# Performance work log

Measured on AMD Instinct MI355X. Metric: run time of the kernel, lower is better.

Reference implementation:

```python
import jax, jax.numpy as jnp
import numpy as np

B, N, F0 = 256, 256, 128
LAYER_SIZES = [128, 128, 128]


def setup_inputs() -> dict:
    key = jax.random.key(0)
    ks = jax.random.split(key, 10)
    x = jax.random.normal(ks[0], (B, N, F0), dtype=jnp.float32)
    adj = jax.random.uniform(ks[1], (B, N, N), dtype=jnp.float32)
    adj = 0.5 * (adj + jnp.swapaxes(adj, -1, -2))  # symmetric weighted adjacency
    f0, f1, f2 = LAYER_SIZES
    W1 = jax.random.normal(ks[2], (f0, f1), dtype=jnp.float32) / np.sqrt(f0)
    b1 = jnp.zeros((f1,), dtype=jnp.float32)
    W2 = jax.random.normal(ks[3], (f1, f2), dtype=jnp.float32) / np.sqrt(f1)
    b2 = jnp.zeros((f2,), dtype=jnp.float32)
    Wr = jax.random.normal(ks[4], (2 * f2, f2), dtype=jnp.float32) / np.sqrt(2 * f2)
    br = jnp.zeros((f2,), dtype=jnp.float32)
    return {"x": x, "adj": adj, "W1": W1, "b1": b1, "W2": W2, "b2": b2, "Wr": Wr, "br": br}


def _normalize_adj(adj):
    # DenseGCNConv: set self-loops (diag=1), then D^{-1/2} (A+I) D^{-1/2} with deg clamped to >=1
    n = adj.shape[-1]
    eye = jnp.eye(n, dtype=adj.dtype)
    a = adj * (1.0 - eye) + eye
    d = jnp.maximum(a.sum(axis=-1), 1.0) ** -0.5  # [B, N]
    return d[..., :, None] * a * d[..., None, :]


def reference(x, adj, W1, b1, W2, b2, Wr, br):
    a = _normalize_adj(adj)  # same adj for both layers; normalization is identical per layer
    h = jnp.einsum("bnm,bmf->bnf", a, x @ W1) + b1  # DenseGCNConv layer 1
    h = jnp.einsum("bnm,bmf->bnf", a, h @ W2) + b2  # DenseGCNConv layer 2
    pooled = jnp.concatenate([h.mean(axis=1), h.max(axis=1)], axis=-1)  # [B, 2F]
    return pooled @ Wr + br  # [B, F]
```

## Files before the change

### kernel.cpp

```cpp
#include <hip/hip_runtime.h>
#include <cstddef>


typedef __attribute__((ext_vector_type(8))) short short8;
typedef __attribute__((ext_vector_type(4))) float f32x4;

static __device__ __forceinline__ unsigned short f2bf(float f) {
  unsigned int u = __float_as_uint(f);
  u += 0x7FFFu + ((u >> 16) & 1u);
  return (unsigned short)(u >> 16);
}

static __device__ __forceinline__ f32x4 mfma16(short8 a, short8 b, f32x4 c) {
  return __builtin_amdgcn_mfma_f32_16x16x32_bf16(a, b, c, 0, 0, 0);
}

static __device__ __forceinline__ int byteT(int f, int k) {
  return ((f << 9) + (k << 1)) ^ ((f & 7) << 4);
}
static __device__ __forceinline__ int byteH(int n, int k) {
  return ((n << 8) + (k << 1)) ^ ((n & 7) << 4);
}

__global__ __launch_bounds__(256) void k_deg_conv(
    const float* __restrict__ adj, unsigned short* __restrict__ Abf,
    float* __restrict__ dinv) {
  const int wid = (blockIdx.x << 2) + (threadIdx.x >> 6);
  const int t = threadIdx.x & 63;
  const int row0 = wid << 3;
  const size_t base0 = (size_t)row0 * 256;
  const int c0 = 4 * t;

  float4 v[8];
  #pragma unroll
  for (int r = 0; r < 8; ++r)
    v[r] = *reinterpret_cast<const float4*>(adj + base0 + (size_t)r * 256 + c0);

  float s[8];
  #pragma unroll
  for (int r = 0; r < 8; ++r) {
    const int n = (row0 + r) & 255;
    v[r].x = (n == c0 + 0) ? 1.0f : v[r].x;
    v[r].y = (n == c0 + 1) ? 1.0f : v[r].y;
    v[r].z = (n == c0 + 2) ? 1.0f : v[r].z;
    v[r].w = (n == c0 + 3) ? 1.0f : v[r].w;
    s[r] = (v[r].x + v[r].y) + (v[r].z + v[r].w);
  }
  #pragma unroll
  for (int off = 32; off >= 1; off >>= 1) {
    #pragma unroll
    for (int r = 0; r < 8; ++r) s[r] += __shfl_xor(s[r], off);
  }

  float sel = s[0];
  #pragma unroll
  for (int r = 1; r < 8; ++r) sel = (t == r) ? s[r] : sel;
  if (t < 8) dinv[row0 + t] = rsqrtf(fmaxf(sel, 1.0f));

  #pragma unroll
  for (int r = 0; r < 8; ++r) {
    ushort4 o;
    o.x = f2bf(v[r].x); o.y = f2bf(v[r].y);
    o.z = f2bf(v[r].z); o.w = f2bf(v[r].w);
    *reinterpret_cast<ushort4*>(Abf + base0 + (size_t)r * 256 + c0) = o;
  }
}

__global__ __launch_bounds__(64) void k_packW2(
    const float* __restrict__ W1, const float* __restrict__ W2,
    unsigned short* __restrict__ P1, unsigned short* __restrict__ P2) {
  const float* W = (blockIdx.x < 32) ? W1 : W2;
  unsigned short* P = (blockIdx.x < 32) ? P1 : P2;
  const int bb = blockIdx.x & 31;
  const int ks = bb >> 3;
  const int r = bb & 7;
  const int l = threadIdx.x;
  const int col = r * 16 + (l & 15);
  const int k0 = ks * 32 + ((l >> 4) << 3);
  short8 frag;
  #pragma unroll
  for (int j = 0; j < 8; ++j)
    frag[j] = (short)f2bf(W[(size_t)(k0 + j) * 128 + col]);
  *reinterpret_cast<short8*>(P + ((size_t)((ks * 8 + r) * 64 + l)) * 8) = frag;
}

__global__ __launch_bounds__(512) void k_fused(
    const unsigned short* __restrict__ Abf, const float* __restrict__ x,
    const unsigned short* __restrict__ W1p, const unsigned short* __restrict__ W2p,
    const float* __restrict__ b1, const float* __restrict__ b2,
    const float* __restrict__ Wr, const float* __restrict__ br,
    const float* __restrict__ dinv, float* __restrict__ out) {
  __shared__ __align__(16) char bufA[65536];
  __shared__ __align__(16) char bufB[65536];
  __shared__ float dinv_s[256];

  const int b = blockIdx.x;
  const int tid = threadIdx.x;
  const int w = tid >> 6;
  const int l = tid & 63;
  const int l15 = l & 15;
  const int khalf = (l >> 4) << 3;
  const int qbase = (l >> 4) << 2;
  const int m = (w << 4) + l15;
  const unsigned short* Ab = Abf + ((size_t)b << 16);
  const int n0w = w << 5;

  float4 xa[4];
  {
    const float* xr = x + ((((size_t)b << 8) + m) << 7);
    #pragma unroll
    for (int k = 0; k < 2; ++k) {
      xa[2 * k]     = *reinterpret_cast<const float4*>(xr + (k << 5) + khalf);
      xa[2 * k + 1] = *reinterpret_cast<const float4*>(xr + (k << 5) + khalf + 4);
    }
  }
  if (tid < 256) dinv_s[tid] = dinv[(b << 8) + tid];
  __syncthreads();

  {
    const short8* Wf = reinterpret_cast<const short8*>(W1p);
    {
      const float* xr = x + ((((size_t)b << 8) + m) << 7);
      float4 xb[4];
      #pragma unroll
      for (int ks = 2; ks < 4; ++ks) {
        xb[2 * (ks - 2)]     = *reinterpret_cast<const float4*>(xr + (ks << 5) + khalf);
        xb[2 * (ks - 2) + 1] = *reinterpret_cast<const float4*>(xr + (ks << 5) + khalf + 4);
      }
      f32x4 acc[8];
      #pragma unroll
      for (int r = 0; r < 8; ++r) acc[r] = (f32x4)(0.0f);
      #pragma unroll
      for (int ks = 0; ks < 4; ++ks) {
        const float4 u = (ks < 2) ? xa[2 * ks] : xb[2 * (ks - 2)];
        const float4 vv = (ks < 2) ? xa[2 * ks + 1] : xb[2 * (ks - 2) + 1];
        short8 bf;
        bf[0] = (short)f2bf(u.x);  bf[1] = (short)f2bf(u.y);
        bf[2] = (short)f2bf(u.z);  bf[3] = (short)f2bf(u.w);
        bf[4] = (short)f2bf(vv.x); bf[5] = (short)f2bf(vv.y);
        bf[6] = (short)f2bf(vv.z); bf[7] = (short)f2bf(vv.w);
        #pragma unroll
        for (int r = 0; r < 8; ++r)
          acc[r] = mfma16(Wf[((ks << 3) + r) * 64 + l], bf, acc[r]);
      }
      const float sc = dinv_s[m];
      #pragma unroll
      for (int r = 0; r < 8; ++r)
        #pragma unroll
        for (int q = 0; q < 4; ++q)
          *reinterpret_cast<unsigned short*>(bufA + byteT((r << 4) + qbase + q, m)) =
              f2bf(acc[r][q] * sc);
    }
    {
      const int m1 = m + 128;
      const float* xr = x + ((((size_t)b << 8) + m1) << 7);
      float4 xc[8];
      #pragma unroll
      for (int ks = 0; ks < 4; ++ks) {
        xc[2 * ks]     = *reinterpret_cast<const float4*>(xr + (ks << 5) + khalf);
        xc[2 * ks + 1] = *reinterpret_cast<const float4*>(xr + (ks << 5) + khalf + 4);
      }
      f32x4 acc[8];
      #pragma unroll
      for (int r = 0; r < 8; ++r) acc[r] = (f32x4)(0.0f);
      #pragma unroll
      for (int ks = 0; ks < 4; ++ks) {
        const float4 u = xc[2 * ks], vv = xc[2 * ks + 1];
        short8 bf;
        bf[0] = (short)f2bf(u.x);  bf[1] = (short)f2bf(u.y);
        bf[2] = (short)f2bf(u.z);  bf[3] = (short)f2bf(u.w);
        bf[4] = (short)f2bf(vv.x); bf[5] = (short)f2bf(vv.y);
        bf[6] = (short)f2bf(vv.z); bf[7] = (short)f2bf(vv.w);
        #pragma unroll
        for (int r = 0; r < 8; ++r)
          acc[r] = mfma16(Wf[((ks << 3) + r) * 64 + l], bf, acc[r]);
      }
      const float sc = dinv_s[m1];
      #pragma unroll
      for (int r = 0; r < 8; ++r)
        #pragma unroll
        for (int q = 0; q < 4; ++q)
          *reinterpret_cast<unsigned short*>(bufA + byteT((r << 4) + qbase + q, m1)) =
              f2bf(acc[r][q] * sc);
    }
  }
  __syncthreads();

  {
    float bs[8];
    #pragma unroll
    for (int c = 0; c < 8; ++c) bs[c] = b1[(c << 4) + l15];
    #pragma unroll
    for (int rt = 0; rt < 2; ++rt) {
      const int nb = n0w + (rt << 4);
      short8 af[8];
      #pragma unroll
      for (int ks = 0; ks < 8; ++ks)
        af[ks] = *reinterpret_cast<const short8*>(
            Ab + (size_t)(nb + l15) * 256 + (ks << 5) + khalf);
      f32x4 acc[8];
      #pragma unroll
      for (int c = 0; c < 8; ++c) acc[c] = (f32x4)(0.0f);
      #pragma unroll
      for (int ks = 0; ks < 8; ++ks) {
        const int k0 = (ks << 5) + khalf;
        #pragma unroll
        for (int c = 0; c < 8; ++c) {
          short8 bf = *reinterpret_cast<const short8*>(bufA + byteT((c << 4) + l15, k0));
          acc[c] = mfma16(af[ks], bf, acc[c]);
        }
      }
      #pragma unroll
      for (int q = 0; q < 4; ++q) {
        const int n = nb + qbase + q;
        const float dv = dinv_s[n];
        #pragma unroll
        for (int c = 0; c < 8; ++c)
          *reinterpret_cast<unsigned short*>(bufB + byteH(n, (c << 4) + l15)) =
              f2bf(acc[c][q] * dv + bs[c]);
      }
    }
  }
  __syncthreads();

  {
    const short8* Wf = reinterpret_cast<const short8*>(W2p);
    #pragma unroll
    for (int p = 0; p < 2; ++p) {
      const int mp = (p << 7) + m;
      f32x4 acc[8];
      #pragma unroll
      for (int r = 0; r < 8; ++r) acc[r] = (f32x4)(0.0f);
      #pragma unroll
      for (int ks = 0; ks < 4; ++ks) {
        const int kk = (ks << 5) + khalf;
        short8 hf = *reinterpret_cast<const short8*>(bufB + byteH(mp, kk));
        #pragma unroll
        for (int r = 0; r < 8; ++r)
          acc[r] = mfma16(Wf[((ks << 3) + r) * 64 + l], hf, acc[r]);
      }
      const float sc = dinv_s[mp];
      #pragma unroll
      for (int r = 0; r < 8; ++r)
        #pragma unroll
        for (int q = 0; q < 4; ++q)
          *reinterpret_cast<unsigned short*>(bufA + byteT((r << 4) + qbase + q, mp)) =
              f2bf(acc[r][q] * sc);
    }
  }
  __syncthreads();

  {
    float bs[8], psum[8], pmax[8];
    #pragma unroll
    for (int c = 0; c < 8; ++c) {
      bs[c] = b2[(c << 4) + l15];
      psum[c] = 0.0f; pmax[c] = -1e30f;
    }
    #pragma unroll
    for (int rt = 0; rt < 2; ++rt) {
      const int nb = n0w + (rt << 4);
      short8 af[8];
      #pragma unroll
      for (int ks = 0; ks < 8; ++ks)
        af[ks] = *reinterpret_cast<const short8*>(
            Ab + (size_t)(nb + l15) * 256 + (ks << 5) + khalf);
      f32x4 acc[8];
      #pragma unroll
      for (int c = 0; c < 8; ++c) acc[c] = (f32x4)(0.0f);
      #pragma unroll
      for (int ks = 0; ks < 8; ++ks) {
        const int k0 = (ks << 5) + khalf;
        #pragma unroll
        for (int c = 0; c < 8; ++c) {
          short8 bf = *reinterpret_cast<const short8*>(bufA + byteT((c << 4) + l15, k0));
          acc[c] = mfma16(af[ks], bf, acc[c]);
        }
      }
      #pragma unroll
      for (int q = 0; q < 4; ++q) {
        const int n = nb + qbase + q;
        const float dv = dinv_s[n];
        #pragma unroll
        for (int c = 0; c < 8; ++c) {
          const float v = acc[c][q] * dv + bs[c];
          psum[c] += v;
          pmax[c] = fmaxf(pmax[c], v);
        }
      }
    }
    #pragma unroll
    for (int c = 0; c < 8; ++c) {
      psum[c] += __shfl_xor(psum[c], 16);
      pmax[c] = fmaxf(pmax[c], __shfl_xor(pmax[c], 16));
      psum[c] += __shfl_xor(psum[c], 32);
      pmax[c] = fmaxf(pmax[c], __shfl_xor(pmax[c], 32));
    }
    float* lds_sum = reinterpret_cast<float*>(bufB);
    float* lds_max = lds_sum + 1024;
    float* pooled  = lds_max + 1024;
    float* rp      = pooled + 256;
    if (l < 16) {
      #pragma unroll
      for (int c = 0; c < 8; ++c) {
        lds_sum[(w << 7) + (c << 4) + l] = psum[c];
        lds_max[(w << 7) + (c << 4) + l] = pmax[c];
      }
    }
    __syncthreads();
    if (tid < 128) {
      float s = 0.0f;
      #pragma unroll
      for (int ww = 0; ww < 8; ++ww) s += lds_sum[(ww << 7) + tid];
      pooled[tid] = s * (1.0f / 256.0f);
    } else if (tid < 256) {
      const int f = tid & 127;
      float mx = -1e30f;
      #pragma unroll
      for (int ww = 0; ww < 8; ++ww) mx = fmaxf(mx, lds_max[(ww << 7) + f]);
      pooled[128 + f] = mx;
    }
    __syncthreads();
    {
      const int f = tid & 127, part = tid >> 7;
      const int base = part << 6;
      float o0 = 0.f, o1 = 0.f;
      #pragma unroll 4
      for (int i = 0; i < 64; i += 2) {
        o0 = fmaf(pooled[base + i],     Wr[(base + i) * 128 + f],     o0);
        o1 = fmaf(pooled[base + i + 1], Wr[(base + i + 1) * 128 + f], o1);
      }
      rp[(part << 7) + f] = o0 + o1;
    }
    __syncthreads();
    if (tid < 128) {
      out[(b << 7) + tid] =
          ((rp[tid] + rp[128 + tid]) + (rp[256 + tid] + rp[384 + tid])) + br[tid];
    }
  }
}

extern "C" void kernel_launch(void* const* d_in, const int* in_sizes, int n_in,
                              void* d_out, int out_size, void* d_ws, size_t ws_size,
                              hipStream_t stream) {
  const float* x   = (const float*)d_in[0];
  const float* adj = (const float*)d_in[1];
  const float* W1  = (const float*)d_in[2];
  const float* b1  = (const float*)d_in[3];
  const float* W2  = (const float*)d_in[4];
  const float* b2  = (const float*)d_in[5];
  const float* Wr  = (const float*)d_in[6];
  const float* br  = (const float*)d_in[7];
  float* out = (float*)d_out;

  char* ws = (char*)d_ws;
  unsigned short* Abf  = (unsigned short*)(ws);
  float*          dinv = (float*)(ws + 33554432);
  unsigned short* W1p  = (unsigned short*)(ws + 33816576);
  unsigned short* W2p  = (unsigned short*)(ws + 33849344);

  k_packW2<<<64, 64, 0, stream>>>(W1, W2, W1p, W2p);
  k_deg_conv<<<2048, 256, 0, stream>>>(adj, Abf, dinv);
  k_fused<<<256, 512, 0, stream>>>(Abf, x, W1p, W2p, b1, b2, Wr, br, dinv, out);
}
```

Before: 63.58 us.

## Split fused GCN kernel into per-layer kernels with two blocks per graph

Replaces the single fused kernel (one 512-thread block per graph, 128KB LDS) with two layer kernels that each use two blocks per graph, each block covering half of the output rows. The hidden layer H1 is written to global memory in bf16, and a third small kernel combines the partial mean/max pooling and applies the readout. The aim is to double the block count to 512 and cut LDS per block to 64KB so more blocks fit per CU. The cost is two extra launches, a global round-trip for H1 and the pooling partials, and the X·W projection being recomputed by both halves.

```diff
diff --git a/kernel.cpp b/kernel.cpp
--- a/kernel.cpp
+++ b/kernel.cpp
@@ -17,9 +17,6 @@
 
 static __device__ __forceinline__ int byteT(int f, int k) {
   return ((f << 9) + (k << 1)) ^ ((f & 7) << 4);
-}
-static __device__ __forceinline__ int byteH(int n, int k) {
-  return ((n << 8) + (k << 1)) ^ ((n & 7) << 4);
 }
 
 __global__ __launch_bounds__(256) void k_deg_conv(
@@ -84,17 +81,15 @@
   *reinterpret_cast<short8*>(P + ((size_t)((ks * 8 + r) * 64 + l)) * 8) = frag;
 }
 
-__global__ __launch_bounds__(512) void k_fused(
+__global__ __launch_bounds__(512, 4) void k_layer1(
     const unsigned short* __restrict__ Abf, const float* __restrict__ x,
-    const unsigned short* __restrict__ W1p, const unsigned short* __restrict__ W2p,
-    const float* __restrict__ b1, const float* __restrict__ b2,
-    const float* __restrict__ Wr, const float* __restrict__ br,
-    const float* __restrict__ dinv, float* __restrict__ out) {
-  __shared__ __align__(16) char bufA[65536];
-  __shared__ __align__(16) char bufB[65536];
+    const unsigned short* __restrict__ W1p, const float* __restrict__ b1,
+    const float* __restrict__ dinv, unsigned short* __restrict__ H1) {
+  __shared__ __align__(16) char bufT[65536];
   __shared__ float dinv_s[256];
 
-  const int b = blockIdx.x;
+  const int b = blockIdx.x >> 1;
+  const int half = blockIdx.x & 1;
   const int tid = threadIdx.x;
   const int w = tid >> 6;
   const int l = tid & 63;
@@ -103,57 +98,16 @@
   const int qbase = (l >> 4) << 2;
   const int m = (w << 4) + l15;
   const unsigned short* Ab = Abf + ((size_t)b << 16);
-  const int n0w = w << 5;
-
-  float4 xa[4];
-  {
-    const float* xr = x + ((((size_t)b << 8) + m) << 7);
-    #pragma unroll
-    for (int k = 0; k < 2; ++k) {
-      xa[2 * k]     = *reinterpret_cast<const float4*>(xr + (k << 5) + khalf);
-      xa[2 * k + 1] = *reinterpret_cast<const float4*>(xr + (k << 5) + khalf + 4);
-    }
-  }
+
   if (tid < 256) dinv_s[tid] = dinv[(b << 8) + tid];
   __syncthreads();
 
   {
     const short8* Wf = reinterpret_cast<const short8*>(W1p);
-    {
-      const float* xr = x + ((((size_t)b << 8) + m) << 7);
-      float4 xb[4];
-      #pragma unroll
-      for (int ks = 2; ks < 4; ++ks) {
-        xb[2 * (ks - 2)]     = *reinterpret_cast<const float4*>(xr + (ks << 5) + khalf);
-        xb[2 * (ks - 2) + 1] = *reinterpret_cast<const float4*>(xr + (ks << 5) + khalf + 4);
-      }
-      f32x4 acc[8];
-      #pragma unroll
-      for (int r = 0; r < 8; ++r) acc[r] = (f32x4)(0.0f);
-      #pragma unroll
-      for (int ks = 0; ks < 4; ++ks) {
-        const float4 u = (ks < 2) ? xa[2 * ks] : xb[2 * (ks - 2)];
-        const float4 vv = (ks < 2) ? xa[2 * ks + 1] : xb[2 * (ks - 2) + 1];
-        short8 bf;
-        bf[0] = (short)f2bf(u.x);  bf[1] = (short)f2bf(u.y);
-        bf[2] = (short)f2bf(u.z);  bf[3] = (short)f2bf(u.w);
-        bf[4] = (short)f2bf(vv.x); bf[5] = (short)f2bf(vv.y);
-        bf[6] = (short)f2bf(vv.z); bf[7] = (short)f2bf(vv.w);
-        #pragma unroll
-        for (int r = 0; r < 8; ++r)
-          acc[r] = mfma16(Wf[((ks << 3) + r) * 64 + l], bf, acc[r]);
-      }
-      const float sc = dinv_s[m];
-      #pragma unroll
-      for (int r = 0; r < 8; ++r)
-        #pragma unroll
-        for (int q = 0; q < 4; ++q)
-          *reinterpret_cast<unsigned short*>(bufA + byteT((r << 4) + qbase + q, m)) =
-              f2bf(acc[r][q] * sc);
-    }
-    {
-      const int m1 = m + 128;
-      const float* xr = x + ((((size_t)b << 8) + m1) << 7);
+    #pragma unroll
+    for (int p = 0; p < 2; ++p) {
+      const int mp = (p << 7) + m;
+      const float* xr = x + ((((size_t)b << 8) + mp) << 7);
       float4 xc[8];
       #pragma unroll
       for (int ks = 0; ks < 4; ++ks) {
@@ -175,12 +129,12 @@
         for (int r = 0; r < 8; ++r)
           acc[r] = mfma16(Wf[((ks << 3) + r) * 64 + l], bf, acc[r]);
       }
-      const float sc = dinv_s[m1];
+      const float sc = dinv_s[mp];
       #pragma unroll
       for (int r = 0; r < 8; ++r)
         #pragma unroll
         for (int q = 0; q < 4; ++q)
-          *reinterpret_cast<unsigned short*>(bufA + byteT((r << 4) + qbase + q, m1)) =
+          *reinterpret_cast<unsigned short*>(bufT + byteT((r << 4) + qbase + q, mp)) =
               f2bf(acc[r][q] * sc);
     }
   }
@@ -190,37 +144,58 @@
     float bs[8];
     #pragma unroll
     for (int c = 0; c < 8; ++c) bs[c] = b1[(c << 4) + l15];
-    #pragma unroll
-    for (int rt = 0; rt < 2; ++rt) {
-      const int nb = n0w + (rt << 4);
-      short8 af[8];
-      #pragma unroll
-      for (int ks = 0; ks < 8; ++ks)
-        af[ks] = *reinterpret_cast<const short8*>(
-            Ab + (size_t)(nb + l15) * 256 + (ks << 5) + khalf);
-      f32x4 acc[8];
-      #pragma unroll
-      for (int c = 0; c < 8; ++c) acc[c] = (f32x4)(0.0f);
-      #pragma unroll
-      for (int ks = 0; ks < 8; ++ks) {
-        const int k0 = (ks << 5) + khalf;
-        #pragma unroll
-        for (int c = 0; c < 8; ++c) {
-          short8 bf = *reinterpret_cast<const short8*>(bufA + byteT((c << 4) + l15, k0));
-          acc[c] = mfma16(af[ks], bf, acc[c]);
-        }
-      }
-      #pragma unroll
-      for (int q = 0; q < 4; ++q) {
-        const int n = nb + qbase + q;
-        const float dv = dinv_s[n];
-        #pragma unroll
-        for (int c = 0; c < 8; ++c)
-          *reinterpret_cast<unsigned short*>(bufB + byteH(n, (c << 4) + l15)) =
-              f2bf(acc[c][q] * dv + bs[c]);
-      }
-    }
-  }
+    const int nb = (half << 7) + (w << 4);
+    short8 af[8];
+    #pragma unroll
+    for (int ks = 0; ks < 8; ++ks)
+      af[ks] = *reinterpret_cast<const short8*>(
+          Ab + (size_t)(nb + l15) * 256 + (ks << 5) + khalf);
+    f32x4 acc[8];
+    #pragma unroll
+    for (int c = 0; c < 8; ++c) acc[c] = (f32x4)(0.0f);
+    #pragma unroll
+    for (int ks = 0; ks < 8; ++ks) {
+      const int k0 = (ks << 5) + khalf;
+      #pragma unroll
+      for (int c = 0; c < 8; ++c) {
+        short8 bf = *reinterpret_cast<const short8*>(bufT + byteT((c << 4) + l15, k0));
+        acc[c] = mfma16(af[ks], bf, acc[c]);
+      }
+    }
+    #pragma unroll
+    for (int q = 0; q < 4; ++q) {
+      const int n = nb + qbase + q;
+      const float dv = dinv_s[n];
+      #pragma unroll
+      for (int c = 0; c < 8; ++c)
+        H1[(((size_t)(b << 8) + n) << 7) + (c << 4) + l15] =
+            f2bf(acc[c][q] * dv + bs[c]);
+    }
+  }
+}
+
+__global__ __launch_bounds__(512, 4) void k_layer2(
+    const unsigned short* __restrict__ Abf, const unsigned short* __restrict__ H1,
+    const unsigned short* __restrict__ W2p, const float* __restrict__ b2,
+    const float* __restrict__ dinv, float* __restrict__ pp) {
+  __shared__ __align__(16) char bufT[65536];
+  __shared__ float lds_sum[8][128];
+  __shared__ float lds_max[8][128];
+  __shared__ float dinv_s[256];
+
+  const int b = blockIdx.x >> 1;
+  const int half = blockIdx.x & 1;
+  const int tid = threadIdx.x;
+  const int w = tid >> 6;
+  const int l = tid & 63;
+  const int l15 = l & 15;
+  const int khalf = (l >> 4) << 3;
+  const int qbase = (l >> 4) << 2;
+  const int m = (w << 4) + l15;
+  const unsigned short* Ab = Abf + ((size_t)b << 16);
+  const unsigned short* Hb = H1 + ((size_t)b << 15);
+
+  if (tid < 256) dinv_s[tid] = dinv[(b << 8) + tid];
   __syncthreads();
 
   {
@@ -234,7 +209,7 @@
       #pragma unroll
       for (int ks = 0; ks < 4; ++ks) {
         const int kk = (ks << 5) + khalf;
-        short8 hf = *reinterpret_cast<const short8*>(bufB + byteH(mp, kk));
+        short8 hf = *reinterpret_cast<const short8*>(Hb + ((size_t)mp << 7) + kk);
         #pragma unroll
         for (int r = 0; r < 8; ++r)
           acc[r] = mfma16(Wf[((ks << 3) + r) * 64 + l], hf, acc[r]);
@@ -244,7 +219,7 @@
       for (int r = 0; r < 8; ++r)
         #pragma unroll
         for (int q = 0; q < 4; ++q)
-          *reinterpret_cast<unsigned short*>(bufA + byteT((r << 4) + qbase + q, mp)) =
+          *reinterpret_cast<unsigned short*>(bufT + byteT((r << 4) + qbase + q, mp)) =
               f2bf(acc[r][q] * sc);
     }
   }
@@ -257,36 +232,33 @@
       bs[c] = b2[(c << 4) + l15];
       psum[c] = 0.0f; pmax[c] = -1e30f;
     }
-    #pragma unroll
-    for (int rt = 0; rt < 2; ++rt) {
-      const int nb = n0w + (rt << 4);
-      short8 af[8];
-      #pragma unroll
-      for (int ks = 0; ks < 8; ++ks)
-        af[ks] = *reinterpret_cast<const short8*>(
-            Ab + (size_t)(nb + l15) * 256 + (ks << 5) + khalf);
-      f32x4 acc[8];
-      #pragma unroll
-      for (int c = 0; c < 8; ++c) acc[c] = (f32x4)(0.0f);
-      #pragma unroll
-      for (int ks = 0; ks < 8; ++ks) {
-        const int k0 = (ks << 5) + khalf;
-        #pragma unroll
-        for (int c = 0; c < 8; ++c) {
-          short8 bf = *reinterpret_cast<const short8*>(bufA + byteT((c << 4) + l15, k0));
-          acc[c] = mfma16(af[ks], bf, acc[c]);
-        }
-      }
-      #pragma unroll
-      for (int q = 0; q < 4; ++q) {
-        const int n = nb + qbase + q;
-        const float dv = dinv_s[n];
-        #pragma unroll
-        for (int c = 0; c < 8; ++c) {
-          const float v = acc[c][q] * dv + bs[c];
-          psum[c] += v;
-          pmax[c] = fmaxf(pmax[c], v);
-        }
+    const int nb = (half << 7) + (w << 4);
+    short8 af[8];
+    #pragma unroll
+    for (int ks = 0; ks < 8; ++ks)
+      af[ks] = *reinterpret_cast<const short8*>(
+          Ab + (size_t)(nb + l15) * 256 + (ks << 5) + khalf);
+    f32x4 acc[8];
+    #pragma unroll
+    for (int c = 0; c < 8; ++c) acc[c] = (f32x4)(0.0f);
+    #pragma unroll
+    for (int ks = 0; ks < 8; ++ks) {
+      const int k0 = (ks << 5) + khalf;
+      #pragma unroll
+      for (int c = 0; c < 8; ++c) {
+        short8 bf = *reinterpret_cast<const short8*>(bufT + byteT((c << 4) + l15, k0));
+        acc[c] = mfma16(af[ks], bf, acc[c]);
+      }
+    }
+    #pragma unroll
+    for (int q = 0; q < 4; ++q) {
+      const int n = nb + qbase + q;
+      const float dv = dinv_s[n];
+      #pragma unroll
+      for (int c = 0; c < 8; ++c) {
+        const float v = acc[c][q] * dv + bs[c];
+        psum[c] += v;
+        pmax[c] = fmaxf(pmax[c], v);
       }
     }
     #pragma unroll
@@ -296,48 +268,62 @@
       psum[c] += __shfl_xor(psum[c], 32);
       pmax[c] = fmaxf(pmax[c], __shfl_xor(pmax[c], 32));
     }
-    float* lds_sum = reinterpret_cast<float*>(bufB);
-    float* lds_max = lds_sum + 1024;
-    float* pooled  = lds_max + 1024;
-    float* rp      = pooled + 256;
     if (l < 16) {
       #pragma unroll
       for (int c = 0; c < 8; ++c) {
-        lds_sum[(w << 7) + (c << 4) + l] = psum[c];
-        lds_max[(w << 7) + (c << 4) + l] = pmax[c];
+        lds_sum[w][(c << 4) + l] = psum[c];
+        lds_max[w][(c << 4) + l] = pmax[c];
       }
     }
     __syncthreads();
     if (tid < 128) {
       float s = 0.0f;
       #pragma unroll
-      for (int ww = 0; ww < 8; ++ww) s += lds_sum[(ww << 7) + tid];
-      pooled[tid] = s * (1.0f / 256.0f);
+      for (int ww = 0; ww < 8; ++ww) s += lds_sum[ww][tid];
+      pp[((size_t)blockIdx.x << 8) + tid] = s;
     } else if (tid < 256) {
       const int f = tid & 127;
       float mx = -1e30f;
       #pragma unroll
-      for (int ww = 0; ww < 8; ++ww) mx = fmaxf(mx, lds_max[(ww << 7) + f]);
-      pooled[128 + f] = mx;
-    }
-    __syncthreads();
-    {
-      const int f = tid & 127, part = tid >> 7;
-      const int base = part << 6;
-      float o0 = 0.f, o1 = 0.f;
-      #pragma unroll 4
-      for (int i = 0; i < 64; i += 2) {
-        o0 = fmaf(pooled[base + i],     Wr[(base + i) * 128 + f],     o0);
-        o1 = fmaf(pooled[base + i + 1], Wr[(base + i + 1) * 128 + f], o1);
-      }
-      rp[(part << 7) + f] = o0 + o1;
-    }
-    __syncthreads();
-    if (tid < 128) {
-      out[(b << 7) + tid] =
-          ((rp[tid] + rp[128 + tid]) + (rp[256 + tid] + rp[384 + tid])) + br[tid];
-    }
-  }
+      for (int ww = 0; ww < 8; ++ww) mx = fmaxf(mx, lds_max[ww][f]);
+      pp[((size_t)blockIdx.x << 8) + 128 + f] = mx;
+    }
+  }
+}
+
+__global__ __launch_bounds__(256) void k_pool(
+    const float* __restrict__ pp, const float* __restrict__ Wr,
+    const float* __restrict__ br, float* __restrict__ out) {
+  __shared__ float pooled[256];
+  __shared__ float rp[256];
+
+  const int b = blockIdx.x;
+  const int tid = threadIdx.x;
+  const float* p0 = pp + ((size_t)(b << 1) << 8);
+  const float* p1 = p0 + 256;
+
+  if (tid < 128) {
+    pooled[tid] = (p0[tid] + p1[tid]) * (1.0f / 256.0f);
+  } else {
+    const int f = tid & 127;
+    pooled[128 + f] = fmaxf(p0[128 + f], p1[128 + f]);
+  }
+  __syncthreads();
+
+  {
+    const int f = tid & 127, part = tid >> 7;
+    const int base = part << 7;
+    float o0 = 0.f, o1 = 0.f;
+    #pragma unroll 4
+    for (int i = 0; i < 128; i += 2) {
+      o0 = fmaf(pooled[base + i],     Wr[(base + i) * 128 + f],     o0);
+      o1 = fmaf(pooled[base + i + 1], Wr[(base + i + 1) * 128 + f], o1);
+    }
+    rp[(part << 7) + f] = o0 + o1;
+  }
+  __syncthreads();
+  if (tid < 128)
+    out[(b << 7) + tid] = rp[tid] + rp[128 + tid] + br[tid];
 }
 
 extern "C" void kernel_launch(void* const* d_in, const int* in_sizes, int n_in,
@@ -355,11 +341,15 @@
 
   char* ws = (char*)d_ws;
   unsigned short* Abf  = (unsigned short*)(ws);
-  float*          dinv = (float*)(ws + 33554432);
-  unsigned short* W1p  = (unsigned short*)(ws + 33816576);
-  unsigned short* W2p  = (unsigned short*)(ws + 33849344);
+  unsigned short* H1   = (unsigned short*)(ws + 33554432);
+  float*          dinv = (float*)(ws + 50331648);
+  float*          pp   = (float*)(ws + 50593792);
+  unsigned short* W1p  = (unsigned short*)(ws + 51118080);
+  unsigned short* W2p  = (unsigned short*)(ws + 51150848);
 
   k_packW2<<<64, 64, 0, stream>>>(W1, W2, W1p, W2p);
   k_deg_conv<<<2048, 256, 0, stream>>>(adj, Abf, dinv);
-  k_fused<<<256, 512, 0, stream>>>(Abf, x, W1p, W2p, b1, b2, Wr, br, dinv, out);
-}
+  k_layer1<<<512, 512, 0, stream>>>(Abf, x, W1p, b1, dinv, H1);
+  k_layer2<<<512, 512, 0, stream>>>(Abf, H1, W2p, b2, dinv, pp);
+  k_pool<<<256, 256, 0, stream>>>(pp, Wr, br, out);
+}
```

New measurement: 82.82 us. +30.3%, slower.
